# Performance work log

Measured on AMD Instinct MI355X. Metric: run time of the kernel, lower is better.

Reference implementation:

```python
import jax, jax.numpy as jnp
import numpy as np

N_NODES = 100000
N_EDGES = 3200000
STATE_DIM = 128
ACTION_DIM = 8


def _w(key, shape, scale=0.05):
    return (jax.random.normal(key, shape, dtype=jnp.float32) * scale)


def setup_inputs() -> dict:
    key = jax.random.key(0)
    ks = jax.random.split(key, 24)
    x = jax.random.normal(ks[0], (N_NODES, STATE_DIM), dtype=jnp.float32)
    edge_index = jax.random.randint(ks[1], (2, N_EDGES), 0, N_NODES, dtype=jnp.int64)
    inp = {
        "x": x,
        "edge_index": edge_index,
        # GCN layers (weights stored [in, out] so forward is x @ W + b)
        "W1": _w(ks[2], (STATE_DIM, 128)), "b1": jnp.zeros((128,), jnp.float32),
        "W2": _w(ks[3], (128, 128)),       "b2": jnp.zeros((128,), jnp.float32),
        "W3": _w(ks[4], (128, 64)),        "b3": jnp.zeros((64,), jnp.float32),
        # actor MLP 64->128->64->ACTION_DIM + softmax
        "Wa1": _w(ks[5], (64, 128)),  "ba1": jnp.zeros((128,), jnp.float32),
        "Wa2": _w(ks[6], (128, 64)),  "ba2": jnp.zeros((64,), jnp.float32),
        "Wa3": _w(ks[7], (64, ACTION_DIM)), "ba3": jnp.zeros((ACTION_DIM,), jnp.float32),
        # critic MLP 64->128->64->1
        "Wc1": _w(ks[8], (64, 128)),  "bc1": jnp.zeros((128,), jnp.float32),
        "Wc2": _w(ks[9], (128, 64)),  "bc2": jnp.zeros((64,), jnp.float32),
        "Wc3": _w(ks[10], (64, 1)),   "bc3": jnp.zeros((1,), jnp.float32),
    }
    return inp


def _gcn_conv(x, W, b, src, dst, norm):
    # GCNConv: D^{-1/2} (A + I) D^{-1/2} X W + b  (self loops already in src/dst)
    h = x @ W                                   # [N, out]
    msg = h[src] * norm[:, None]                # gather + per-edge scale
    agg = jax.ops.segment_sum(msg, dst, num_segments=N_NODES)
    return agg + b


def reference(x, edge_index,
              W1, b1, W2, b2, W3, b3,
              Wa1, ba1, Wa2, ba2, Wa3, ba3,
              Wc1, bc1, Wc2, bc2, Wc3, bc3):
    loop = jnp.arange(N_NODES, dtype=edge_index.dtype)
    src = jnp.concatenate([edge_index[0], loop])
    dst = jnp.concatenate([edge_index[1], loop])
    deg = jax.ops.segment_sum(jnp.ones_like(dst, dtype=x.dtype), dst,
                              num_segments=N_NODES)
    dinv = jax.lax.rsqrt(deg)                   # deg >= 1 via self loops
    norm = dinv[src] * dinv[dst]                # [E+N]

    # forward_gnn (dropout is identity in eval mode)
    h = jax.nn.relu(_gcn_conv(x, W1, b1, src, dst, norm))
    h = jax.nn.relu(_gcn_conv(h, W2, b2, src, dst, norm))
    h = _gcn_conv(h, W3, b3, src, dst, norm)    # [N, 64]

    a = jax.nn.relu(h @ Wa1 + ba1)
    a = jax.nn.relu(a @ Wa2 + ba2)
    probs = jax.nn.softmax(a @ Wa3 + ba3, axis=-1)   # [N, ACTION_DIM]

    c = jax.nn.relu(h @ Wc1 + bc1)
    c = jax.nn.relu(c @ Wc2 + bc2)
    values = c @ Wc3 + bc3                      # [N, 1]

    return jnp.concatenate([probs, values], axis=-1)  # [N, ACTION_DIM+1]
```

## Files before the change

kernel.cpp:

```cpp
#include <hip/hip_runtime.h>
#include <hip/hip_bf16.h>
#include <math.h>


#define WS_ALIGN(x) (((x) + 255) & ~(size_t)255)

constexpr int RNG  = 64;
constexpr int NRG  = 1563;
constexpr int NB   = 1024;
constexpr int CHK  = 16;

constexpr float S_FP8     = 64.0f;
constexpr float S_FP8_INV = 1.0f / 64.0f;

using bf16x8 = __attribute__((ext_vector_type(8))) short;
using f32x4  = __attribute__((ext_vector_type(4))) float;
using f32x2  = __attribute__((ext_vector_type(2))) float;

__device__ __forceinline__ float b2f(unsigned short u) {
    return __uint_as_float(((unsigned int)u) << 16);
}
__device__ __forceinline__ unsigned short f2b(float f) {
    __hip_bfloat16 hb = __float2bfloat16(f);
    return *(unsigned short*)&hb;
}
__device__ __forceinline__ unsigned char f2fp8(float f) {
    return (unsigned char)(__builtin_amdgcn_cvt_pk_fp8_f32(f, f, 0, false) & 0xff);
}
__device__ __forceinline__ int pad8(int v) { return (v + 7) & ~7; }

__device__ __forceinline__ void acc8(uint2 u, f32x2& a01, f32x2& a23,
                                     f32x2& a45, f32x2& a67) {
    a01 += __builtin_amdgcn_cvt_pk_f32_fp8((int)u.x, false);
    a23 += __builtin_amdgcn_cvt_pk_f32_fp8((int)u.x, true);
    a45 += __builtin_amdgcn_cvt_pk_f32_fp8((int)u.y, false);
    a67 += __builtin_amdgcn_cvt_pk_f32_fp8((int)u.y, true);
}


__global__ __launch_bounds__(256) void bucket_count_k(
    const int* __restrict__ dst, int* __restrict__ bcnt, int E,
    const float* __restrict__ W1, const float* __restrict__ W2,
    const float* __restrict__ W3, const float* __restrict__ Wa1,
    const float* __restrict__ Wc1, const float* __restrict__ Wa2,
    const float* __restrict__ Wc2, unsigned short* __restrict__ wt) {
    __shared__ int c64[RNG];
    int b = blockIdx.x, t = threadIdx.x;

    int gi = b * 256 + t;
    if (gi < 73728) {
        const float* W; int off, K, OUT;
        if (gi < 16384)      { W = W1;  off = 0;     K = 128; OUT = 128; }
        else if (gi < 32768) { W = W2;  off = 16384; K = 128; OUT = 128; }
        else if (gi < 40960) { W = W3;  off = 32768; K = 128; OUT = 64; }
        else if (gi < 49152) { W = Wa1; off = 40960; K = 64;  OUT = 128; }
        else if (gi < 57344) { W = Wc1; off = 49152; K = 64;  OUT = 128; }
        else if (gi < 65536) { W = Wa2; off = 57344; K = 128; OUT = 64; }
        else                 { W = Wc2; off = 65536; K = 128; OUT = 64; }
        int j = gi - off, k = j / OUT, n = j - k * OUT;
        wt[off + n * K + k] = f2b(W[j]);
    }

    if (t < RNG) c64[t] = 0;
    __syncthreads();
    int ec = (E + NB - 1) / NB;
    int e0 = b * ec, e1 = min(E, e0 + ec);
    for (int e = e0 + t; e < e1; e += 256) {
        int d = __builtin_nontemporal_load(dst + e);
        atomicAdd(&c64[d / NRG], 1);
    }
    __syncthreads();
    if (t < RNG) bcnt[t * NB + b] = c64[t];
}

__global__ __launch_bounds__(256) void rsum_k(
    const int* __restrict__ bcnt, int* __restrict__ base, int* __restrict__ rtot) {
    __shared__ int s[256];
    int r = blockIdx.x, t = threadIdx.x;
    const int* row = bcnt + (size_t)r * NB;
    int v[4], loc = 0;
#pragma unroll
    for (int j = 0; j < 4; j++) { v[j] = row[t * 4 + j]; loc += v[j]; }
    s[t] = loc;
    __syncthreads();
    for (int d = 1; d < 256; d <<= 1) {
        int x = (t >= d) ? s[t - d] : 0;
        __syncthreads();
        s[t] += x;
        __syncthreads();
    }
    int run = s[t] - loc;
    int* bp = base + (size_t)r * NB + t * 4;
#pragma unroll
    for (int j = 0; j < 4; j++) { bp[j] = run; run += v[j]; }
    if (t == 255) rtot[r] = s[255];
}

__global__ __launch_bounds__(256) void bucket_scatter_k(
    const int* __restrict__ src, const int* __restrict__ dst,
    const int* __restrict__ base, const int* __restrict__ rtot,
    unsigned* __restrict__ bucket, int E) {
    __shared__ int cur[RNG];
    __shared__ int rt[RNG];
    int b = blockIdx.x, t = threadIdx.x;
    if (t < RNG) rt[t] = rtot[t];
    __syncthreads();
    if (t < RNG) {
        int run = 0;
        for (int j = 0; j < t; j++) run += rt[j];
        cur[t] = run + base[(size_t)t * NB + b];
    }
    __syncthreads();
    int ec = (E + NB - 1) / NB;
    int e0 = b * ec, e1 = min(E, e0 + ec);
    for (int e = e0 + t; e < e1; e += 256) {
        int d = __builtin_nontemporal_load(dst + e);
        int sv = __builtin_nontemporal_load(src + e);
        int r = d / NRG;
        int pos = atomicAdd(&cur[r], 1);
        bucket[pos] = ((unsigned)(d - r * NRG) << 17) | (unsigned)sv;
    }
}

__global__ __launch_bounds__(256) void hist_bucket_k(
    const unsigned* __restrict__ bucket, const int* __restrict__ rtot,
    int* __restrict__ hist) {
    __shared__ int h[NRG];
    __shared__ int ss[2];
    int b = blockIdx.x, r = b & 63, c2 = b >> 6, t = threadIdx.x;
    for (int i = t; i < NRG; i += 256) h[i] = 0;
    if (t == 0) {
        int run = 0;
        for (int j = 0; j < r; j++) run += rtot[j];
        ss[0] = run; ss[1] = run + rtot[r];
    }
    __syncthreads();
    int s0 = ss[0], s1 = ss[1];
    int ec = (s1 - s0 + CHK - 1) / CHK;
    int e0 = s0 + c2 * ec, e1 = min(s1, e0 + ec);
    for (int e = e0 + t; e < e1; e += 256) {
        unsigned v = __builtin_nontemporal_load(bucket + e);
        atomicAdd(&h[v >> 17], 1);
    }
    __syncthreads();
    int* out = hist + ((size_t)r * CHK + c2) * NRG;
    for (int i = t; i < NRG; i += 256) out[i] = h[i];
}

__global__ __launch_bounds__(256) void sum_hist_dinv_k(
    const int* __restrict__ hist, int* __restrict__ cnt,
    float* __restrict__ dinv, int* __restrict__ bsum, int N) {
    __shared__ int sd[256];
    int t = threadIdx.x;
    int i = blockIdx.x * 256 + t;
    int s = 0;
    if (i < N) {
        int r = i / NRG, li = i - r * NRG;
        const int* hp = hist + ((size_t)r * CHK) * NRG + li;
#pragma unroll
        for (int c = 0; c < CHK; c++) s += hp[(size_t)c * NRG];
        cnt[i] = s;
        dinv[i] = rsqrtf((float)s + 1.0f);
    }
    sd[t] = (i < N) ? pad8(s) : 0;
    __syncthreads();
    for (int d = 128; d > 0; d >>= 1) {
        if (t < d) sd[t] += sd[t + d];
        __syncthreads();
    }
    if (t == 0) bsum[blockIdx.x] = sd[0];
}

__global__ void scan_off_pad_k(const int* __restrict__ cnt, const int* __restrict__ bsum,
                               int* __restrict__ rowptr, int* __restrict__ hist,
                               int* __restrict__ col, int N) {
    __shared__ int s[256];
    int t = threadIdx.x, b = blockIdx.x;

    int part = 0;
    for (int j = t; j < b; j += 256) part += bsum[j];
    s[t] = part;
    __syncthreads();
    for (int d = 128; d > 0; d >>= 1) {
        if (t < d) s[t] += s[t + d];
        __syncthreads();
    }
    int boffv = s[0];
    __syncthreads();

    int i = b * 256 + t;
    int cv = (i < N) ? cnt[i] : 0;
    int v = pad8(cv);
    if (i >= N) v = 0;
    s[t] = v;
    __syncthreads();
    for (int d = 1; d < 256; d <<= 1) {
        int x = (t >= d) ? s[t - d] : 0;
        __syncthreads();
        s[t] += x;
        __syncthreads();
    }
    if (b == (int)gridDim.x - 1 && t == 255) rowptr[N] = boffv + s[255];
    if (i < N) {
        int rp = s[t] - v + boffv;
        rowptr[i] = rp;
        int r = i / NRG, li = i - r * NRG;
        int* hp = hist + ((size_t)r * CHK) * NRG + li;
        int run = rp;
#pragma unroll
        for (int c = 0; c < CHK; c++) {
            int hv = hp[(size_t)c * NRG];
            hp[(size_t)c * NRG] = run;
            run += hv;
        }
        for (int e = rp + cv; e < rp + v; e++) col[e] = N;
    }
}

__global__ __launch_bounds__(256) void fill2_k(
    const unsigned* __restrict__ bucket, const int* __restrict__ rtot,
    const int* __restrict__ hist, int* __restrict__ col) {
    __shared__ int cur[NRG];
    __shared__ int ss[2];
    int b = blockIdx.x, r = b & 63, c2 = b >> 6, t = threadIdx.x;
    const int* hp = hist + ((size_t)r * CHK + c2) * NRG;
    for (int i = t; i < NRG; i += 256) cur[i] = hp[i];
    if (t == 0) {
        int run = 0;
        for (int j = 0; j < r; j++) run += rtot[j];
        ss[0] = run; ss[1] = run + rtot[r];
    }
    __syncthreads();
    int s0 = ss[0], s1 = ss[1];
    int ec = (s1 - s0 + CHK - 1) / CHK;
    int e0 = s0 + c2 * ec, e1 = min(s1, e0 + ec);
    for (int e = e0 + t; e < e1; e += 256) {
        unsigned v = __builtin_nontemporal_load(bucket + e);
        int slot = atomicAdd(&cur[v >> 17], 1);
        col[slot] = (int)(v & 0x1FFFFu);
    }
}


template <int K, int OUT, int EPI, bool AF32>
__global__ __launch_bounds__(256) void gemm2_k(
    const void* __restrict__ Xv, int ldx, const unsigned short* __restrict__ Wt,
    const float* __restrict__ sb, const float* __restrict__ w3b,
    const float* __restrict__ b3, void* __restrict__ Yv, int N, int NT) {
    constexpr int LDK = K + 8;
    __shared__ __align__(16) unsigned short Bs[OUT * LDK];
    __shared__ __align__(16) unsigned short As[64 * LDK];
    int t = threadIdx.x;

    for (int g = t; g < OUT * (K / 8); g += 256) {
        int r = g / (K / 8), q = g - r * (K / 8);
        *(uint4*)&Bs[r * LDK + q * 8] = *(const uint4*)(Wt + r * K + q * 8);
    }

    int wv = t >> 6, lane = t & 63;
    int lm = lane & 15, lq = lane >> 4;
    constexpr int CT = OUT / 16;

    for (int tile = blockIdx.x; tile < NT; tile += gridDim.x) {
        int rowBase = tile * 64;

        if constexpr (AF32) {
            const float* X = (const float*)Xv;
            for (int g = t; g < 64 * (K / 8); g += 256) {
                int r = g / (K / 8), q = g - r * (K / 8);
                int gr = rowBase + r;
                unsigned short us[8];
                if (gr < N) {
                    float4 v0 = *(const float4*)(X + (size_t)gr * ldx + q * 8);
                    float4 v1 = *(const float4*)(X + (size_t)gr * ldx + q * 8 + 4);
                    us[0] = f2b(v0.x); us[1] = f2b(v0.y); us[2] = f2b(v0.z); us[3] = f2b(v0.w);
                    us[4] = f2b(v1.x); us[5] = f2b(v1.y); us[6] = f2b(v1.z); us[7] = f2b(v1.w);
                } else {
#pragma unroll
                    for (int j = 0; j < 8; j++) us[j] = 0;
                }
                *(uint4*)&As[r * LDK + q * 8] = *(uint4*)us;
            }
        } else {
            const unsigned short* X = (const unsigned short*)Xv;
            for (int g = t; g < 64 * (K / 8); g += 256) {
                int r = g / (K / 8), q = g - r * (K / 8);
                int gr = rowBase + r;
                uint4 v = make_uint4(0, 0, 0, 0);
                if (gr < N) v = *(const uint4*)(X + (size_t)gr * ldx + q * 8);
                *(uint4*)&As[r * LDK + q * 8] = v;
            }
        }
        __syncthreads();

        f32x4 acc[CT];
#pragma unroll
        for (int c = 0; c < CT; c++) acc[c] = (f32x4){0.f, 0.f, 0.f, 0.f};

        const unsigned short* arow = &As[(wv * 16 + lm) * LDK + lq * 8];
#pragma unroll
        for (int kt = 0; kt < K / 32; kt++) {
            bf16x8 a = *(const bf16x8*)(arow + kt * 32);
#pragma unroll
            for (int c = 0; c < CT; c++) {
                bf16x8 b = *(const bf16x8*)&Bs[(c * 16 + lm) * LDK + kt * 32 + lq * 8];
                acc[c] = __builtin_amdgcn_mfma_f32_16x16x32_bf16(a, b, acc[c], 0, 0, 0);
            }
        }

        int r0 = rowBase + wv * 16 + lq * 4;
        if constexpr (EPI == 0) {
#pragma unroll
            for (int r = 0; r < 4; r++) {
                int gr = r0 + r;
                float scale = (gr < N) ? sb[gr] * S_FP8 : 0.f;
#pragma unroll
                for (int c = 0; c < CT; c++) {
                    int colg = c * 16 + lm;
                    ((unsigned char*)Yv)[(size_t)gr * OUT + colg] = f2fp8(acc[c][r] * scale);
                }
            }
        }
        __syncthreads();
    }
}


template <bool RELU>
__global__ __launch_bounds__(256) void agg128_k(
    const unsigned char* __restrict__ H,
    const int* __restrict__ rowptr, const int* __restrict__ col,
    const float* __restrict__ dinv, const float* __restrict__ bias,
    unsigned short* __restrict__ Y, int N, int Ecap) {
    int tid = threadIdx.x;
    int node = blockIdx.x * 4 + (tid >> 6);
    if (node >= N) return;
    int lane = tid & 63;
    int grp = lane >> 4;
    int li8 = (lane & 15) * 8;

    f32x2 a01 = {0.f, 0.f}, a23 = {0.f, 0.f}, a45 = {0.f, 0.f}, a67 = {0.f, 0.f};
    if (grp == 0) {
        uint2 u = *(const uint2*)(H + (size_t)node * 128 + li8);
        acc8(u, a01, a23, a45, a67);
    }

    int start = rowptr[node], end = rowptr[node + 1];
    for (int e0 = start; e0 < end; e0 += 64) {
        int cv = col[min(e0 + lane, Ecap - 1)];
        int quads = min(64, end - e0) >> 2;
        for (int q = 0; q < quads; q += 2) {
            int s0 = __shfl(cv, 4 * q + grp, 64);
            int s1 = __shfl(cv, 4 * q + 4 + grp, 64);
            uint2 u0 = *(const uint2*)(H + (size_t)s0 * 128 + li8);
            uint2 u1 = *(const uint2*)(H + (size_t)s1 * 128 + li8);
            acc8(u0, a01, a23, a45, a67);
            acc8(u1, a01, a23, a45, a67);
        }
    }

#pragma unroll
    for (int w = 16; w < 64; w <<= 1) {
        a01[0] += __shfl_xor(a01[0], w, 64); a01[1] += __shfl_xor(a01[1], w, 64);
        a23[0] += __shfl_xor(a23[0], w, 64); a23[1] += __shfl_xor(a23[1], w, 64);
        a45[0] += __shfl_xor(a45[0], w, 64); a45[1] += __shfl_xor(a45[1], w, 64);
        a67[0] += __shfl_xor(a67[0], w, 64); a67[1] += __shfl_xor(a67[1], w, 64);
    }

    if (grp == 0) {
        float dv = dinv[node] * S_FP8_INV;
        float4 b0 = *(const float4*)(bias + li8);
        float4 b1 = *(const float4*)(bias + li8 + 4);
        float o0 = a01[0] * dv + b0.x, o1 = a01[1] * dv + b0.y;
        float o2 = a23[0] * dv + b0.z, o3 = a23[1] * dv + b0.w;
        float o4 = a45[0] * dv + b1.x, o5 = a45[1] * dv + b1.y;
        float o6 = a67[0] * dv + b1.z, o7 = a67[1] * dv + b1.w;
        if (RELU) {
            o0 = fmaxf(o0, 0.f); o1 = fmaxf(o1, 0.f); o2 = fmaxf(o2, 0.f); o3 = fmaxf(o3, 0.f);
            o4 = fmaxf(o4, 0.f); o5 = fmaxf(o5, 0.f); o6 = fmaxf(o6, 0.f); o7 = fmaxf(o7, 0.f);
        }
        unsigned short us[8] = {f2b(o0), f2b(o1), f2b(o2), f2b(o3),
                                f2b(o4), f2b(o5), f2b(o6), f2b(o7)};
        *(uint4*)(Y + (size_t)node * 128 + li8) = *(uint4*)us;
    }
}

__global__ __launch_bounds__(256) void agg64_k(
    const unsigned char* __restrict__ H,
    const int* __restrict__ rowptr, const int* __restrict__ col,
    const float* __restrict__ dinv, const float* __restrict__ bias,
    unsigned short* __restrict__ Y, int N, int Ecap) {
    int tid = threadIdx.x;
    int node = blockIdx.x * 4 + (tid >> 6);
    if (node >= N) return;
    int lane = tid & 63;
    int grp = lane >> 3;
    int li8 = (lane & 7) * 8;

    f32x2 a01 = {0.f, 0.f}, a23 = {0.f, 0.f}, a45 = {0.f, 0.f}, a67 = {0.f, 0.f};
    if (grp == 0) {
        uint2 u = *(const uint2*)(H + (size_t)node * 64 + li8);
        acc8(u, a01, a23, a45, a67);
    }

    int start = rowptr[node], end = rowptr[node + 1];
    for (int e0 = start; e0 < end; e0 += 64) {
        int cv = col[min(e0 + lane, Ecap - 1)];
        int octs = min(64, end - e0) >> 3;
        int o = 0;
        for (; o + 2 <= octs; o += 2) {
            int s0 = __shfl(cv, 8 * o + grp, 64);
            int s1 = __shfl(cv, 8 * o + 8 + grp, 64);
            uint2 u0 = *(const uint2*)(H + (size_t)s0 * 64 + li8);
            uint2 u1 = *(const uint2*)(H + (size_t)s1 * 64 + li8);
            acc8(u0, a01, a23, a45, a67);
            acc8(u1, a01, a23, a45, a67);
        }
        if (o < octs) {
            int s0 = __shfl(cv, 8 * o + grp, 64);
            uint2 u0 = *(const uint2*)(H + (size_t)s0 * 64 + li8);
            acc8(u0, a01, a23, a45, a67);
        }
    }

#pragma unroll
    for (int w = 8; w < 64; w <<= 1) {
        a01[0] += __shfl_xor(a01[0], w, 64); a01[1] += __shfl_xor(a01[1], w, 64);
        a23[0] += __shfl_xor(a23[0], w, 64); a23[1] += __shfl_xor(a23[1], w, 64);
        a45[0] += __shfl_xor(a45[0], w, 64); a45[1] += __shfl_xor(a45[1], w, 64);
        a67[0] += __shfl_xor(a67[0], w, 64); a67[1] += __shfl_xor(a67[1], w, 64);
    }

    if (grp == 0) {
        float dv = dinv[node] * S_FP8_INV;
        float4 b0 = *(const float4*)(bias + li8);
        float4 b1 = *(const float4*)(bias + li8 + 4);
        unsigned short us[8] = {
            f2b(a01[0] * dv + b0.x), f2b(a01[1] * dv + b0.y),
            f2b(a23[0] * dv + b0.z), f2b(a23[1] * dv + b0.w),
            f2b(a45[0] * dv + b1.x), f2b(a45[1] * dv + b1.y),
            f2b(a67[0] * dv + b1.z), f2b(a67[1] * dv + b1.w)};
        *(uint4*)(Y + (size_t)node * 64 + li8) = *(uint4*)us;
    }
}


__global__ __launch_bounds__(256) void headsB_k(
    const unsigned short* __restrict__ h3,
    const unsigned short* __restrict__ Wh1t,
    const float* __restrict__ ba1, const float* __restrict__ bc1,
    const unsigned short* __restrict__ Wa2t,
    const float* __restrict__ ba2,
    const unsigned short* __restrict__ Wc2t,
    const float* __restrict__ bc2,
    const float* __restrict__ Wa3, const float* __restrict__ ba3,
    const float* __restrict__ Wc3, const float* __restrict__ bc3,
    float* __restrict__ out, int N, int NT, int GH) {
    constexpr int LD64 = 72, LD128 = 136;
    __shared__ __align__(16) unsigned short Bs1[128 * LD64];
    __shared__ __align__(16) unsigned short Bs2[64 * LD128];
    __shared__ __align__(16) unsigned short As[4 * 16 * LD64];
    __shared__ __align__(16) unsigned short A1[4 * 16 * LD128];
    int t = threadIdx.x, wv = t >> 6, lane = t & 63;
    int lm = lane & 15, lq = lane >> 4;

    bool actor = (int)blockIdx.x < GH;
    const unsigned short* W1t = actor ? Wh1t : Wh1t + 128 * 64;
    const float* b1v = actor ? ba1 : bc1;
    const unsigned short* W2t = actor ? Wa2t : Wc2t;
    const float* b2v = actor ? ba2 : bc2;
    const float* w3  = actor ? Wa3 : Wc3;
    const float* b3v = actor ? ba3 : bc3;
    int tile0 = actor ? (int)blockIdx.x : (int)blockIdx.x - GH;

    for (int g = t; g < 128 * 8; g += 256) {
        int r = g >> 3, q = g & 7;
        *(uint4*)&Bs1[r * LD64 + q * 8] = *(const uint4*)(W1t + r * 64 + q * 8);
    }
    for (int g = t; g < 64 * 16; g += 256) {
        int r = g >> 4, q = g & 15;
        *(uint4*)&Bs2[r * LD128 + q * 8] = *(const uint4*)(W2t + r * 128 + q * 8);
    }
    __syncthreads();

    unsigned short* Asw = &As[wv * 16 * LD64];
    unsigned short* A1w = &A1[wv * 16 * LD128];

    for (int tile = tile0; tile < NT; tile += GH) {
        int rowBase = tile * 64 + wv * 16;

        for (int g = lane; g < 16 * 8; g += 64) {
            int r = g >> 3, q = g & 7;
            int gr = rowBase + r;
            uint4 v = make_uint4(0, 0, 0, 0);
            if (gr < N) v = *(const uint4*)(h3 + (size_t)gr * 64 + q * 8);
            *(uint4*)&Asw[r * LD64 + q * 8] = v;
        }

        f32x4 acc1[8];
#pragma unroll
        for (int c = 0; c < 8; c++) acc1[c] = (f32x4){0.f, 0.f, 0.f, 0.f};
        const unsigned short* arow = &Asw[lm * LD64 + lq * 8];
#pragma unroll
        for (int kt = 0; kt < 2; kt++) {
            bf16x8 a = *(const bf16x8*)(arow + kt * 32);
#pragma unroll
            for (int c = 0; c < 8; c++) {
                bf16x8 b = *(const bf16x8*)&Bs1[(c * 16 + lm) * LD64 + kt * 32 + lq * 8];
                acc1[c] = __builtin_amdgcn_mfma_f32_16x16x32_bf16(a, b, acc1[c], 0, 0, 0);
            }
        }
#pragma unroll
        for (int r = 0; r < 4; r++) {
            int lr = lq * 4 + r;
#pragma unroll
            for (int c = 0; c < 8; c++) {
                int colg = c * 16 + lm;
                float v = fmaxf(acc1[c][r] + b1v[colg], 0.f);
                A1w[lr * LD128 + colg] = f2b(v);
            }
        }

        f32x4 acc[4];
#pragma unroll
        for (int c = 0; c < 4; c++) acc[c] = (f32x4){0.f, 0.f, 0.f, 0.f};
        const unsigned short* arow2 = &A1w[lm * LD128 + lq * 8];
#pragma unroll
        for (int kt = 0; kt < 4; kt++) {
            bf16x8 a = *(const bf16x8*)(arow2 + kt * 32);
#pragma unroll
            for (int c = 0; c < 4; c++) {
                bf16x8 b = *(const bf16x8*)&Bs2[(c * 16 + lm) * LD128 + kt * 32 + lq * 8];
                acc[c] = __builtin_amdgcn_mfma_f32_16x16x32_bf16(a, b, acc[c], 0, 0, 0);
            }
        }

        int r0 = rowBase + lq * 4;
        if (actor) {
            float l[4][8];
#pragma unroll
            for (int r = 0; r < 4; r++)
#pragma unroll
                for (int a = 0; a < 8; a++) l[r][a] = 0.f;
#pragma unroll
            for (int c = 0; c < 4; c++) {
                int colg = c * 16 + lm;
#pragma unroll
                for (int r = 0; r < 4; r++) {
                    float v = fmaxf(acc[c][r] + b2v[colg], 0.f);
#pragma unroll
                    for (int a = 0; a < 8; a++)
                        l[r][a] = fmaf(v, w3[colg * 8 + a], l[r][a]);
                }
            }
#pragma unroll
            for (int w = 1; w < 16; w <<= 1)
#pragma unroll
                for (int r = 0; r < 4; r++)
#pragma unroll
                    for (int a = 0; a < 8; a++)
                        l[r][a] += __shfl_xor(l[r][a], w, 64);
            if (lm < 8) {
#pragma unroll
                for (int r = 0; r < 4; r++) {
                    int gr = r0 + r;
                    if (gr < N) {
                        float lg[8], m = -1e30f;
#pragma unroll
                        for (int a = 0; a < 8; a++) { lg[a] = l[r][a] + b3v[a]; m = fmaxf(m, lg[a]); }
                        float sum = 0.f;
#pragma unroll
                        for (int a = 0; a < 8; a++) { lg[a] = expf(lg[a] - m); sum += lg[a]; }
                        out[(size_t)gr * 9 + lm] = lg[lm] / sum;
                    }
                }
            }
        } else {
            float lv[4] = {0.f, 0.f, 0.f, 0.f};
#pragma unroll
            for (int c = 0; c < 4; c++) {
                int colg = c * 16 + lm;
#pragma unroll
                for (int r = 0; r < 4; r++) {
                    float v = fmaxf(acc[c][r] + b2v[colg], 0.f);
                    lv[r] = fmaf(v, w3[colg], lv[r]);
                }
            }
#pragma unroll
            for (int w = 1; w < 16; w <<= 1)
#pragma unroll
                for (int r = 0; r < 4; r++) lv[r] += __shfl_xor(lv[r], w, 64);
            if (lm == 0) {
#pragma unroll
                for (int r = 0; r < 4; r++) {
                    int gr = r0 + r;
                    if (gr < N) out[(size_t)gr * 9 + 8] = lv[r] + b3v[0];
                }
            }
        }
    }
}


extern "C" void kernel_launch(void* const* d_in, const int* in_sizes, int n_in,
                              void* d_out, int out_size, void* d_ws, size_t ws_size,
                              hipStream_t stream) {
    const float* x   = (const float*)d_in[0];
    const int*   ei  = (const int*)d_in[1];
    const float* W1  = (const float*)d_in[2];  const float* b1  = (const float*)d_in[3];
    const float* W2  = (const float*)d_in[4];  const float* b2  = (const float*)d_in[5];
    const float* W3  = (const float*)d_in[6];  const float* b3  = (const float*)d_in[7];
    const float* Wa1 = (const float*)d_in[8];  const float* ba1 = (const float*)d_in[9];
    const float* Wa2 = (const float*)d_in[10]; const float* ba2 = (const float*)d_in[11];
    const float* Wa3 = (const float*)d_in[12]; const float* ba3 = (const float*)d_in[13];
    const float* Wc1 = (const float*)d_in[14]; const float* bc1 = (const float*)d_in[15];
    const float* Wc2 = (const float*)d_in[16]; const float* bc2 = (const float*)d_in[17];
    const float* Wc3 = (const float*)d_in[18]; const float* bc3 = (const float*)d_in[19];
    float* out = (float*)d_out;

    const int N = in_sizes[0] / 128;
    const int E = in_sizes[1] / 2;
    const int* src = ei;
    const int* dst = ei + E;
    const int Ecap = E + 8 * N;
    const int Npad = ((N + 63) / 64) * 64;
    const int NT   = (N + 63) / 64;

    size_t off = 0;
    auto take = [&](size_t bytes) { size_t o = off; off = WS_ALIGN(off + bytes); return o; };
    char* ws = (char*)d_ws;
    unsigned short* h3     = (unsigned short*)(ws + take((size_t)N * 64 * 2));
    unsigned short* h      = (unsigned short*)(ws + take((size_t)N * 128 * 2));
    unsigned char*  hpr8   = (unsigned char*) (ws + take((size_t)(Npad + 64) * 128));
    int*            col    = (int*)(ws + take((size_t)Ecap * 4));
    unsigned short* wt     = (unsigned short*)(ws + take(73728 * 2));
    float* dinv   = (float*)(ws + take((size_t)(N + 64) * 4));
    int*   cnt    = (int*)  (ws + take((size_t)N * 4));
    int*   rowptr = (int*)  (ws + take((size_t)(N + 1) * 4));
    int*   bcnt   = (int*)  (ws + take((size_t)RNG * NB * 4));
    int*   base   = (int*)  (ws + take((size_t)RNG * NB * 4));
    int*   rtot   = (int*)  (ws + take(RNG * 4));
    int*   bsum   = (int*)  (ws + take(512 * 4));
    unsigned* bucket = (unsigned*)h;
    int* hist = (int*)h3;
    (void)ws_size; (void)n_in; (void)out_size;

    const int nb  = (N + 255) / 256;
    const int GG128 = 768;
    const int GG64  = 1024;
    const int GH    = 512;

    const unsigned short* W1t  = wt;
    const unsigned short* W2t  = wt + 16384;
    const unsigned short* W3t  = wt + 32768;
    const unsigned short* Wh1t = wt + 40960;
    const unsigned short* Wa2t = wt + 57344;
    const unsigned short* Wc2t = wt + 65536;

    bucket_count_k<<<NB, 256, 0, stream>>>(dst, bcnt, E,
                                           W1, W2, W3, Wa1, Wc1, Wa2, Wc2, wt);
    rsum_k<<<RNG, 256, 0, stream>>>(bcnt, base, rtot);
    bucket_scatter_k<<<NB, 256, 0, stream>>>(src, dst, base, rtot, bucket, E);
    hist_bucket_k<<<RNG * CHK, 256, 0, stream>>>(bucket, rtot, hist);
    sum_hist_dinv_k<<<nb, 256, 0, stream>>>(hist, cnt, dinv, bsum, N);
    scan_off_pad_k<<<nb, 256, 0, stream>>>(cnt, bsum, rowptr, hist, col, N);
    fill2_k<<<RNG * CHK, 256, 0, stream>>>(bucket, rtot, hist, col);

    gemm2_k<128, 128, 0, true><<<GG128, 256, 0, stream>>>(
        x, 128, W1t, dinv, nullptr, nullptr, hpr8, N, NT);
    agg128_k<true><<<(N + 3) / 4, 256, 0, stream>>>(hpr8, rowptr, col, dinv, b1, h, N, Ecap);
    gemm2_k<128, 128, 0, false><<<GG128, 256, 0, stream>>>(
        h, 128, W2t, dinv, nullptr, nullptr, hpr8, N, NT);
    agg128_k<true><<<(N + 3) / 4, 256, 0, stream>>>(hpr8, rowptr, col, dinv, b2, h, N, Ecap);
    gemm2_k<128, 64, 0, false><<<GG64, 256, 0, stream>>>(
        h, 128, W3t, dinv, nullptr, nullptr, hpr8, N, NT);
    agg64_k<<<(N + 3) / 4, 256, 0, stream>>>(hpr8, rowptr, col, dinv, b3, h3, N, Ecap);

    headsB_k<<<2 * GH, 256, 0, stream>>>(
        h3, Wh1t, ba1, bc1, Wa2t, ba2, Wc2t, bc2, Wa3, ba3, Wc3, bc3, out, N, NT, GH);
}
```

Baseline: 462.7 us.

## Permute feature columns so GEMM epilogue writes packed fp8 vectors

The GEMM epilogue now packs each lane's per-tile fp8 outputs into one 8-byte (or 4-byte) store instead of issuing separate byte stores at strided columns. This stores features in a permuted column order. To stay consistent, the downstream weight rows (W2, W3, Wa1, Wc1) and the biases b1-b3 are permuted the same way during setup. This cuts store instruction count and uncoalesced byte writes in the GEMM, at the cost of a permuted intermediate layout that every consumer must agree on.

```diff
diff --git a/kernel.cpp b/kernel.cpp
--- a/kernel.cpp
+++ b/kernel.cpp
@@ -43,22 +43,32 @@
     const float* __restrict__ W1, const float* __restrict__ W2,
     const float* __restrict__ W3, const float* __restrict__ Wa1,
     const float* __restrict__ Wc1, const float* __restrict__ Wa2,
-    const float* __restrict__ Wc2, unsigned short* __restrict__ wt) {
+    const float* __restrict__ Wc2,
+    const float* __restrict__ b1, const float* __restrict__ b2,
+    const float* __restrict__ b3,
+    unsigned short* __restrict__ wt, float* __restrict__ bp) {
     __shared__ int c64[RNG];
     int b = blockIdx.x, t = threadIdx.x;
 
     int gi = b * 256 + t;
     if (gi < 73728) {
-        const float* W; int off, K, OUT;
+        const float* W; int off, K, OUT; int pm = 0;
         if (gi < 16384)      { W = W1;  off = 0;     K = 128; OUT = 128; }
-        else if (gi < 32768) { W = W2;  off = 16384; K = 128; OUT = 128; }
-        else if (gi < 40960) { W = W3;  off = 32768; K = 128; OUT = 64; }
-        else if (gi < 49152) { W = Wa1; off = 40960; K = 64;  OUT = 128; }
-        else if (gi < 57344) { W = Wc1; off = 49152; K = 64;  OUT = 128; }
+        else if (gi < 32768) { W = W2;  off = 16384; K = 128; OUT = 128; pm = 1; }
+        else if (gi < 40960) { W = W3;  off = 32768; K = 128; OUT = 64;  pm = 1; }
+        else if (gi < 49152) { W = Wa1; off = 40960; K = 64;  OUT = 128; pm = 2; }
+        else if (gi < 57344) { W = Wc1; off = 49152; K = 64;  OUT = 128; pm = 2; }
         else if (gi < 65536) { W = Wa2; off = 57344; K = 128; OUT = 64; }
         else                 { W = Wc2; off = 65536; K = 128; OUT = 64; }
         int j = gi - off, k = j / OUT, n = j - k * OUT;
-        wt[off + n * K + k] = f2b(W[j]);
+        int kp = (pm == 1) ? ((k & 15) * 8 + (k >> 4))
+               : (pm == 2) ? ((k & 15) * 4 + (k >> 4)) : k;
+        wt[off + n * K + kp] = f2b(W[j]);
+    } else if (gi < 74048) {
+        int j = gi - 73728;
+        if (j < 128)      bp[(j & 15) * 8 + (j >> 4)] = b1[j];
+        else if (j < 256) { int j2 = j - 128; bp[128 + (j2 & 15) * 8 + (j2 >> 4)] = b2[j2]; }
+        else              { int j3 = j - 256; bp[256 + (j3 & 15) * 4 + (j3 >> 4)] = b3[j3]; }
     }
 
     if (t < RNG) c64[t] = 0;
@@ -90,9 +100,9 @@
         __syncthreads();
     }
     int run = s[t] - loc;
-    int* bp = base + (size_t)r * NB + t * 4;
-#pragma unroll
-    for (int j = 0; j < 4; j++) { bp[j] = run; run += v[j]; }
+    int* bp2 = base + (size_t)r * NB + t * 4;
+#pragma unroll
+    for (int j = 0; j < 4; j++) { bp2[j] = run; run += v[j]; }
     if (t == 255) rtot[r] = s[255];
 }
 
@@ -314,10 +324,18 @@
             for (int r = 0; r < 4; r++) {
                 int gr = r0 + r;
                 float scale = (gr < N) ? sb[gr] * S_FP8 : 0.f;
-#pragma unroll
-                for (int c = 0; c < CT; c++) {
-                    int colg = c * 16 + lm;
-                    ((unsigned char*)Yv)[(size_t)gr * OUT + colg] = f2fp8(acc[c][r] * scale);
+                if constexpr (OUT == 128) {
+                    unsigned w0 = 0, w1 = 0;
+                    w0 = __builtin_amdgcn_cvt_pk_fp8_f32(acc[0][r] * scale, acc[1][r] * scale, w0, false);
+                    w0 = __builtin_amdgcn_cvt_pk_fp8_f32(acc[2][r] * scale, acc[3][r] * scale, w0, true);
+                    w1 = __builtin_amdgcn_cvt_pk_fp8_f32(acc[4][r] * scale, acc[5][r] * scale, w1, false);
+                    w1 = __builtin_amdgcn_cvt_pk_fp8_f32(acc[6][r] * scale, acc[7][r] * scale, w1, true);
+                    *(uint2*)((unsigned char*)Yv + (size_t)gr * 128 + lm * 8) = make_uint2(w0, w1);
+                } else {
+                    unsigned w0 = 0;
+                    w0 = __builtin_amdgcn_cvt_pk_fp8_f32(acc[0][r] * scale, acc[1][r] * scale, w0, false);
+                    w0 = __builtin_amdgcn_cvt_pk_fp8_f32(acc[2][r] * scale, acc[3][r] * scale, w0, true);
+                    *(unsigned*)((unsigned char*)Yv + (size_t)gr * 64 + lm * 4) = w0;
                 }
             }
         }
@@ -634,6 +652,7 @@
     unsigned char*  hpr8   = (unsigned char*) (ws + take((size_t)(Npad + 64) * 128));
     int*            col    = (int*)(ws + take((size_t)Ecap * 4));
     unsigned short* wt     = (unsigned short*)(ws + take(73728 * 2));
+    float* bperm  = (float*)(ws + take(320 * 4));
     float* dinv   = (float*)(ws + take((size_t)(N + 64) * 4));
     int*   cnt    = (int*)  (ws + take((size_t)N * 4));
     int*   rowptr = (int*)  (ws + take((size_t)(N + 1) * 4));
@@ -656,9 +675,13 @@
     const unsigned short* Wh1t = wt + 40960;
     const unsigned short* Wa2t = wt + 57344;
     const unsigned short* Wc2t = wt + 65536;
+    const float* b1p = bperm;
+    const float* b2p = bperm + 128;
+    const float* b3p = bperm + 256;
 
     bucket_count_k<<<NB, 256, 0, stream>>>(dst, bcnt, E,
-                                           W1, W2, W3, Wa1, Wc1, Wa2, Wc2, wt);
+                                           W1, W2, W3, Wa1, Wc1, Wa2, Wc2,
+                                           b1, b2, b3, wt, bperm);
     rsum_k<<<RNG, 256, 0, stream>>>(bcnt, base, rtot);
     bucket_scatter_k<<<NB, 256, 0, stream>>>(src, dst, base, rtot, bucket, E);
     hist_bucket_k<<<RNG * CHK, 256, 0, stream>>>(bucket, rtot, hist);
@@ -668,13 +691,13 @@
 
     gemm2_k<128, 128, 0, true><<<GG128, 256, 0, stream>>>(
         x, 128, W1t, dinv, nullptr, nullptr, hpr8, N, NT);
-    agg128_k<true><<<(N + 3) / 4, 256, 0, stream>>>(hpr8, rowptr, col, dinv, b1, h, N, Ecap);
+    agg128_k<true><<<(N + 3) / 4, 256, 0, stream>>>(hpr8, rowptr, col, dinv, b1p, h, N, Ecap);
     gemm2_k<128, 128, 0, false><<<GG128, 256, 0, stream>>>(
         h, 128, W2t, dinv, nullptr, nullptr, hpr8, N, NT);
-    agg128_k<true><<<(N + 3) / 4, 256, 0, stream>>>(hpr8, rowptr, col, dinv, b2, h, N, Ecap);
+    agg128_k<true><<<(N + 3) / 4, 256, 0, stream>>>(hpr8, rowptr, col, dinv, b2p, h, N, Ecap);
     gemm2_k<128, 64, 0, false><<<GG64, 256, 0, stream>>>(
         h, 128, W3t, dinv, nullptr, nullptr, hpr8, N, NT);
-    agg64_k<<<(N + 3) / 4, 256, 0, stream>>>(hpr8, rowptr, col, dinv, b3, h3, N, Ecap);
+    agg64_k<<<(N + 3) / 4, 256, 0, stream>>>(hpr8, rowptr, col, dinv, b3p, h3, N, Ecap);
 
     headsB_k<<<2 * GH, 256, 0, stream>>>(
         h3, Wh1t, ba1, bc1, Wa2t, ba2, Wc2t, bc2, Wa3, ba3, Wc3, bc3, out, N, NT, GH);
```

Result: no change. 458.9 us, median of 2 (-0.8%).
